# Optimization experiments

Measured on AMD Instinct MI355X. Metric: run time of the kernel, lower is better.

The kernel has to match this reference:

```python
import jax, jax.numpy as jnp
import numpy as np


def _cdist(x, y):
    # Euclidean (L2) distance matrix, matching torch.cdist default p=2.
    # x: [B,N,D], y: [B,M,D] -> [B,N,M]
    x2 = jnp.sum(x * x, axis=-1, keepdims=True)          # [B,N,1]
    y2 = jnp.sum(y * y, axis=-1, keepdims=True)          # [B,M,1]
    d2 = x2 + jnp.swapaxes(y2, -1, -2) - 2.0 * jnp.einsum('bnd,bmd->bnm', x, y)
    return jnp.sqrt(jnp.maximum(d2, 0.0))


def setup_inputs() -> dict:
    key = jax.random.key(0)
    k1, k2, k3 = jax.random.split(key, 3)
    B, N, G, D = 1, 8192, 2048, 64
    expression = jax.random.normal(k1, (B, N, G), dtype=jnp.float32)
    encoding = jax.random.normal(k2, (B, N, D), dtype=jnp.float32)
    quality = jax.random.normal(k3, (B, N, 1), dtype=jnp.float32)
    return {"expression": expression, "encoding": encoding, "quality": quality}


def reference(expression, encoding, quality):
    # scores[b,i,j] = -||enc_i - enc_j|| + quality[b,j]
    scores = -_cdist(encoding, encoding) + jnp.swapaxes(quality, -1, -2)  # [B,N,N]
    similarity = jax.nn.softmax(scores, axis=-1)
    return similarity @ expression  # [B,N,G]
```

## Files before the change

### kernel.cpp

```cpp
#include <hip/hip_runtime.h>
#include <hip/hip_bf16.h>


typedef __attribute__((ext_vector_type(8))) short bf16x8;
typedef __attribute__((ext_vector_type(4))) float f32x4;
typedef __attribute__((ext_vector_type(16))) float f32x16;

constexpr int N_ = 8192;
constexpr int G_ = 2048;
constexpr int D_ = 64;

__device__ __forceinline__ unsigned short f32_to_bf16(float f) {
  unsigned u = __builtin_bit_cast(unsigned, f);
  u = (u + 0x7FFFu + ((u >> 16) & 1u)) >> 16;
  return (unsigned short)u;
}
__device__ __forceinline__ float bf16_to_f32(unsigned short h) {
  unsigned u = ((unsigned)h) << 16;
  return __builtin_bit_cast(float, u);
}

typedef __attribute__((address_space(1))) const unsigned int glob_u32;
typedef __attribute__((address_space(3))) unsigned int lds_u32;
__device__ __forceinline__ void gload_lds16(const void* g, void* l) {
  __builtin_amdgcn_global_load_lds((glob_u32*)g, (lds_u32*)l, 16, 0, 0);
}

__global__ void prep_kernel(const float* __restrict__ enc,
                            const float* __restrict__ quality,
                            float* __restrict__ norms,
                            float2* __restrict__ nq,
                            unsigned short* __restrict__ encb) {
  int row = blockIdx.x * blockDim.x + threadIdx.x;
  if (row >= N_) return;
  const float* r = enc + (size_t)row * D_;
  float n = 0.f;
#pragma unroll
  for (int k = 0; k < D_; k += 4) {
    float4 v = *(const float4*)(r + k);
    n += v.x * v.x + v.y * v.y + v.z * v.z + v.w * v.w;
    ushort4 h;
    h.x = f32_to_bf16(v.x); h.y = f32_to_bf16(v.y);
    h.z = f32_to_bf16(v.z); h.w = f32_to_bf16(v.w);
    *(ushort4*)(encb + (size_t)row * D_ + k) = h;
  }
  norms[row] = n;
  nq[row] = make_float2(n, quality[row]);
}

__global__ void etrans_kernel(const float* __restrict__ E,
                              unsigned short* __restrict__ ET) {
  __shared__ __align__(16) unsigned short t[64 * 72];
  int j0 = blockIdx.x * 64;
  int g0 = blockIdx.y * 64;
  int tid = threadIdx.x;
#pragma unroll
  for (int it = 0; it < 4; ++it) {
    int r = it * 16 + (tid >> 4);
    int c4 = tid & 15;
    float4 v = *(const float4*)(E + (size_t)(j0 + r) * G_ + g0 + c4 * 4);
    t[(c4 * 4 + 0) * 72 + r] = f32_to_bf16(v.x);
    t[(c4 * 4 + 1) * 72 + r] = f32_to_bf16(v.y);
    t[(c4 * 4 + 2) * 72 + r] = f32_to_bf16(v.z);
    t[(c4 * 4 + 3) * 72 + r] = f32_to_bf16(v.w);
  }
  __syncthreads();
#pragma unroll
  for (int it = 0; it < 2; ++it) {
    int g = it * 32 + (tid >> 3);
    int ch = tid & 7;
    bf16x8 v = *(const bf16x8*)(&t[g * 72 + ch * 8]);
    *(bf16x8*)(ET + (size_t)(g0 + g) * N_ + j0 + ch * 8) = v;
  }
}

__global__ __launch_bounds__(256)
void pk_kernel(const unsigned short* __restrict__ encb,
               const float* __restrict__ norms,
               const float2* __restrict__ nq,
               unsigned short* __restrict__ P,
               float* __restrict__ lpart) {
  __shared__ __align__(16) unsigned short p_lds[64 * 72];

  const int tid = threadIdx.x;
  const int wave = tid >> 6;
  const int lane = tid & 63;
  const int quad = lane >> 4;
  const int l15 = lane & 15;

  const int i0 = blockIdx.y * 64;
  const int jbase = blockIdx.x * 1024;
  const int irow_a = i0 + 16 * wave + l15;
  const int iloc_c = 16 * wave + quad * 4;
  const int irow_c = i0 + iloc_c;

  const int srow_loc = 16 * wave + (lane >> 2);

  bf16x8 afrag[2];
#pragma unroll
  for (int ks = 0; ks < 2; ++ks)
    afrag[ks] = *(const bf16x8*)(encb + (size_t)irow_a * 64 + ks * 32 + quad * 8);

  float ni[4];
#pragma unroll
  for (int r = 0; r < 4; ++r) ni[r] = norms[irow_c + r];

  float lsum[4] = {0.f, 0.f, 0.f, 0.f};

  for (int js = 0; js < 16; ++js) {
    const int j0j = jbase + js * 64;
#pragma unroll
    for (int jt = 0; jt < 4; ++jt) {
      const int jrow = j0j + jt * 16 + l15;
      bf16x8 b0 = *(const bf16x8*)(encb + (size_t)jrow * 64 + quad * 8);
      bf16x8 b1 = *(const bf16x8*)(encb + (size_t)jrow * 64 + 32 + quad * 8);
      float2 njq = nq[jrow];
      f32x4 s4 = {0.f, 0.f, 0.f, 0.f};
      s4 = __builtin_amdgcn_mfma_f32_16x16x32_bf16(afrag[0], b0, s4, 0, 0, 0);
      s4 = __builtin_amdgcn_mfma_f32_16x16x32_bf16(afrag[1], b1, s4, 0, 0, 0);
#pragma unroll
      for (int r = 0; r < 4; ++r) {
        float d2 = fmaxf(ni[r] + njq.x - 2.0f * s4[r], 0.f);
        float sc = njq.y - sqrtf(d2);
        if (irow_c + r == jrow) sc = njq.y;
        float p = __expf(sc);
        unsigned short pb = f32_to_bf16(p);
        lsum[r] += bf16_to_f32(pb);
        p_lds[(iloc_c + r) * 72 + jt * 16 + l15] = pb;
      }
    }
    __syncthreads();
#pragma unroll
    for (int k = 0; k < 2; ++k) {
      int c = (lane & 3) + k * 4;
      bf16x8 v = *(const bf16x8*)(&p_lds[srow_loc * 72 + c * 8]);
      *(bf16x8*)(P + (size_t)(i0 + srow_loc) * N_ + j0j + c * 8) = v;
    }
    __syncthreads();
  }
#pragma unroll
  for (int r = 0; r < 4; ++r) {
    float v = lsum[r];
    v += __shfl_xor(v, 1);
    v += __shfl_xor(v, 2);
    v += __shfl_xor(v, 4);
    v += __shfl_xor(v, 8);
    lsum[r] = v;
  }
  if (l15 == 0) {
#pragma unroll
    for (int r = 0; r < 4; ++r)
      lpart[(size_t)blockIdx.x * N_ + irow_c + r] = lsum[r];
  }
}

__global__ void inv_kernel(const float* __restrict__ lpart,
                           float* __restrict__ linv) {
  int i = blockIdx.x * blockDim.x + threadIdx.x;
  if (i >= N_) return;
  float s = 0.f;
#pragma unroll
  for (int c = 0; c < 8; ++c) s += lpart[(size_t)c * N_ + i];
  linv[i] = 1.0f / s;
}

__global__ __launch_bounds__(256, 2)
void gemm_kernel(const unsigned short* __restrict__ P,
                 const unsigned short* __restrict__ ET,
                 const float* __restrict__ linv,
                 float* __restrict__ out) {
  __shared__ __align__(16) unsigned short aT[256 * 64];
  __shared__ __align__(16) unsigned short bT[128 * 64];

  const int tid = threadIdx.x;
  const int wave = tid >> 6;
  const int lane = tid & 63;
  const int quad = lane >> 4;
  const int l15 = lane & 15;

  const int g0 = blockIdx.x * 128;
  const int i0 = blockIdx.y * 256;
  const int wrow = (wave >> 1) * 128;
  const int wcol = (wave & 1) * 64;

  const int strow = tid >> 3;
  const int stc = tid & 7;

  f32x4 acc[8][4];
#pragma unroll
  for (int a = 0; a < 8; ++a)
#pragma unroll
    for (int b = 0; b < 4; ++b) acc[a][b] = (f32x4){0.f, 0.f, 0.f, 0.f};

  for (int kk = 0; kk < N_; kk += 64) {
#pragma unroll
    for (int s = 0; s < 8; ++s) {
      int row = s * 32 + strow;
      int csrc = stc ^ (row & 7);
      gload_lds16(P + (size_t)(i0 + row) * N_ + kk + csrc * 8,
                  &aT[row * 64 + stc * 8]);
    }
#pragma unroll
    for (int s = 0; s < 4; ++s) {
      int row = s * 32 + strow;
      int csrc = stc ^ (row & 7);
      gload_lds16(ET + (size_t)(g0 + row) * N_ + kk + csrc * 8,
                  &bT[row * 64 + stc * 8]);
    }
    __syncthreads();
#pragma unroll
    for (int ks = 0; ks < 2; ++ks) {
      const int swzk = ((ks * 4 + quad) ^ (l15 & 7)) * 8;
      bf16x8 bF[4];
#pragma unroll
      for (int ct = 0; ct < 4; ++ct)
        bF[ct] = *(const bf16x8*)(&bT[(wcol + ct * 16 + l15) * 64 + swzk]);
#pragma unroll
      for (int rt = 0; rt < 8; ++rt) {
        bf16x8 aF = *(const bf16x8*)(&aT[(wrow + rt * 16 + l15) * 64 + swzk]);
#pragma unroll
        for (int ct = 0; ct < 4; ++ct)
          acc[rt][ct] = __builtin_amdgcn_mfma_f32_16x16x32_bf16(aF, bF[ct], acc[rt][ct], 0, 0, 0);
      }
    }
    __syncthreads();
  }

  float li[8];
#pragma unroll
  for (int rt = 0; rt < 8; ++rt) {
    li[rt] = 0.f;
  }
#pragma unroll
  for (int rt = 0; rt < 8; ++rt) {
    float lir[4];
#pragma unroll
    for (int r = 0; r < 4; ++r)
      lir[r] = linv[i0 + wrow + rt * 16 + quad * 4 + r];
#pragma unroll
    for (int ct = 0; ct < 4; ++ct)
#pragma unroll
      for (int r = 0; r < 4; ++r) {
        int row = wrow + rt * 16 + quad * 4 + r;
        int col = wcol + ct * 16 + l15;
        out[(size_t)(i0 + row) * G_ + g0 + col] = acc[rt][ct][r] * lir[r];
      }
  }
}

__global__ __launch_bounds__(256, 2)
void fused_kernel(const unsigned short* __restrict__ encb,
                  const float* __restrict__ norms,
                  const float2* __restrict__ nq,
                  const unsigned short* __restrict__ ET,
                  float* __restrict__ out) {
  __shared__ __align__(16) unsigned short p_lds[128 * 72];
  __shared__ __align__(16) unsigned short e_lds[256 * 72];
  __shared__ float linv_lds[128];

  const int tid = threadIdx.x;
  const int wave = tid >> 6;
  const int lane = tid & 63;
  const int quad = lane >> 4;
  const int l15 = lane & 15;
  const int half = lane >> 5;
  const int l31 = lane & 31;

  const int gt = blockIdx.x & 7;
  const int it = blockIdx.x >> 3;
  const int i0 = it * 128;
  const int g0 = gt * 256;

  const int srow = 32 * wave;
  const int wr = wave >> 1, wc = wave & 1;
  const int prow = 64 * wr;
  const int pcol = 128 * wc;

  bf16x8 afrag[2][2];
#pragma unroll
  for (int rt = 0; rt < 2; ++rt)
#pragma unroll
    for (int ks = 0; ks < 2; ++ks)
      afrag[rt][ks] = *(const bf16x8*)(encb +
          (size_t)(i0 + srow + rt * 16 + l15) * 64 + ks * 32 + quad * 8);

  float ni[2][4];
#pragma unroll
  for (int rt = 0; rt < 2; ++rt)
#pragma unroll
    for (int r = 0; r < 4; ++r)
      ni[rt][r] = norms[i0 + srow + rt * 16 + quad * 4 + r];

  float lsum[2][4] = {};
  f32x16 acc[2][4];
#pragma unroll
  for (int a = 0; a < 2; ++a)
#pragma unroll
    for (int b = 0; b < 4; ++b)
#pragma unroll
      for (int e = 0; e < 16; ++e) acc[a][b][e] = 0.f;

  for (int j0j = 0; j0j < N_; j0j += 64) {
#pragma unroll
    for (int s = 0; s < 8; ++s) {
      int g = s * 32 + (tid >> 3);
      int ch = tid & 7;
      bf16x8 v = *(const bf16x8*)(ET + (size_t)(g0 + g) * N_ + j0j + ch * 8);
      *(bf16x8*)(&e_lds[g * 72 + ch * 8]) = v;
    }
#pragma unroll
    for (int jt = 0; jt < 4; ++jt) {
      const int jrow = j0j + jt * 16 + l15;
      bf16x8 b0 = *(const bf16x8*)(encb + (size_t)jrow * 64 + quad * 8);
      bf16x8 b1 = *(const bf16x8*)(encb + (size_t)jrow * 64 + 32 + quad * 8);
      float2 njq = nq[jrow];
#pragma unroll
      for (int rt = 0; rt < 2; ++rt) {
        f32x4 s4 = {0.f, 0.f, 0.f, 0.f};
        s4 = __builtin_amdgcn_mfma_f32_16x16x32_bf16(afrag[rt][0], b0, s4, 0, 0, 0);
        s4 = __builtin_amdgcn_mfma_f32_16x16x32_bf16(afrag[rt][1], b1, s4, 0, 0, 0);
#pragma unroll
        for (int r = 0; r < 4; ++r) {
          int i_loc = srow + rt * 16 + quad * 4 + r;
          float d2 = fmaxf(ni[rt][r] + njq.x - 2.0f * s4[r], 0.f);
          float sc = njq.y - sqrtf(d2);
          if (i0 + i_loc == jrow) sc = njq.y;
          float p = __expf(sc);
          unsigned short pb = f32_to_bf16(p);
          lsum[rt][r] += bf16_to_f32(pb);
          p_lds[i_loc * 72 + jt * 16 + l15] = pb;
        }
      }
    }
    __syncthreads();
#pragma unroll
    for (int ks = 0; ks < 4; ++ks) {
      bf16x8 pa0 = *(const bf16x8*)(&p_lds[(prow + l31) * 72 + ks * 16 + half * 8]);
      bf16x8 pa1 = *(const bf16x8*)(&p_lds[(prow + 32 + l31) * 72 + ks * 16 + half * 8]);
#pragma unroll
      for (int ct = 0; ct < 4; ++ct) {
        bf16x8 eb = *(const bf16x8*)(&e_lds[(pcol + ct * 32 + l31) * 72 + ks * 16 + half * 8]);
        acc[0][ct] = __builtin_amdgcn_mfma_f32_32x32x16_bf16(pa0, eb, acc[0][ct], 0, 0, 0);
        acc[1][ct] = __builtin_amdgcn_mfma_f32_32x32x16_bf16(pa1, eb, acc[1][ct], 0, 0, 0);
      }
    }
    __syncthreads();
  }

#pragma unroll
  for (int rt = 0; rt < 2; ++rt)
#pragma unroll
    for (int r = 0; r < 4; ++r) {
      float v = lsum[rt][r];
      v += __shfl_xor(v, 1);
      v += __shfl_xor(v, 2);
      v += __shfl_xor(v, 4);
      v += __shfl_xor(v, 8);
      lsum[rt][r] = v;
    }
  if (l15 == 0) {
#pragma unroll
    for (int rt = 0; rt < 2; ++rt)
#pragma unroll
      for (int r = 0; r < 4; ++r)
        linv_lds[srow + rt * 16 + quad * 4 + r] = 1.0f / lsum[rt][r];
  }
  __syncthreads();

#pragma unroll
  for (int rt2 = 0; rt2 < 2; ++rt2)
#pragma unroll
    for (int ct = 0; ct < 4; ++ct)
#pragma unroll
      for (int e = 0; e < 16; ++e) {
        int row = prow + rt2 * 32 + (e & 3) + 8 * (e >> 2) + 4 * half;
        int col = pcol + ct * 32 + l31;
        out[(size_t)(i0 + row) * G_ + g0 + col] = acc[rt2][ct][e] * linv_lds[row];
      }
}

extern "C" void kernel_launch(void* const* d_in, const int* in_sizes, int n_in,
                              void* d_out, int out_size, void* d_ws, size_t ws_size,
                              hipStream_t stream) {
  const float* expr = (const float*)d_in[0];
  const float* enc  = (const float*)d_in[1];
  const float* qual = (const float*)d_in[2];
  float* out = (float*)d_out;

  char* ws = (char*)d_ws;
  const size_t off_norms = 0;
  const size_t off_nq    = 32768;
  const size_t off_lpart = 98304;
  const size_t off_linv  = 360448;
  const size_t off_encb  = 393216;
  const size_t off_ET    = 1441792;
  const size_t off_P     = 34996224;
  const size_t need      = off_P + (size_t)N_ * N_ * 2;

  if (ws_size >= need) {
    float* norms         = (float*)(ws + off_norms);
    float2* nqp          = (float2*)(ws + off_nq);
    float* lpart         = (float*)(ws + off_lpart);
    float* linv          = (float*)(ws + off_linv);
    unsigned short* encb = (unsigned short*)(ws + off_encb);
    unsigned short* ET   = (unsigned short*)(ws + off_ET);
    unsigned short* P    = (unsigned short*)(ws + off_P);

    prep_kernel<<<dim3(N_ / 256), dim3(256), 0, stream>>>(enc, qual, norms, nqp, encb);
    etrans_kernel<<<dim3(N_ / 64, G_ / 64), dim3(256), 0, stream>>>(expr, ET);
    pk_kernel<<<dim3(8, N_ / 64), dim3(256), 0, stream>>>(encb, norms, nqp, P, lpart);
    inv_kernel<<<dim3(N_ / 256), dim3(256), 0, stream>>>(lpart, linv);
    gemm_kernel<<<dim3(G_ / 128, N_ / 256), dim3(256), 0, stream>>>(P, ET, linv, out);
  } else {
    float* norms         = (float*)ws;
    float2* nqp          = (float2*)(ws + 32768);
    unsigned short* encb = (unsigned short*)(ws + 98304);
    unsigned short* ET   = (unsigned short*)(ws + 1146880);
    prep_kernel<<<dim3(N_ / 256), dim3(256), 0, stream>>>(enc, qual, norms, nqp, encb);
    etrans_kernel<<<dim3(N_ / 64, G_ / 64), dim3(256), 0, stream>>>(expr, ET);
    fused_kernel<<<dim3((N_ / 128) * (G_ / 256)), dim3(256), 0, stream>>>(encb, norms, nqp, ET, out);
  }
}
```

Measured before the change: 429.6 us.

## Add 256x256-tile 8-wave GEMM with triple-buffered LDS pipeline and swizzled block order

```diff
diff --git a/kernel.cpp b/kernel.cpp
--- a/kernel.cpp
+++ b/kernel.cpp
@@ -164,6 +164,147 @@
   linv[i] = 1.0f / s;
 }
 
+constexpr int GBM = 256, GBN = 256, GBK = 32;
+constexpr int GNT = N_ / GBK;
+constexpr int SLOT_A = GBM * GBK;
+constexpr int SLOT_B = GBN * GBK;
+constexpr int SLOT = SLOT_A + SLOT_B;
+constexpr int GEMM_LDS_BYTES = 3 * SLOT * 2;
+
+__global__ __launch_bounds__(512, 2)
+void gemm8_kernel(const unsigned short* __restrict__ P,
+                  const unsigned short* __restrict__ ET,
+                  const float* __restrict__ linv,
+                  float* __restrict__ out) {
+  extern __shared__ __align__(16) unsigned short smem[];
+
+  const int tid = threadIdx.x;
+  const int wave = tid >> 6;
+  const int lane = tid & 63;
+  const int quad = lane >> 4;
+  const int l15 = lane & 15;
+
+  const int bid = blockIdx.x;
+  const int lg = (bid & 7) * 32 + (bid >> 3);
+  const int gx = lg & 7;
+  const int gy = lg >> 3;
+  const int g0 = gx * GBN;
+  const int i0 = gy * GBM;
+
+  const int wm = wave >> 2;
+  const int wn = wave & 3;
+  const int wrow = wm * 128;
+  const int wcol = wn * 64;
+
+  unsigned short* cur = smem;
+  unsigned short* nxt = smem + SLOT;
+  unsigned short* stg = smem + 2 * SLOT;
+
+  const int strow = tid >> 2;
+  const int stch = tid & 3;
+  const int rowS0 = strow, rowS1 = 128 + strow;
+  const int cs0 = stch ^ ((rowS0 >> 1) & 3);
+  const int cs1 = stch ^ ((rowS1 >> 1) & 3);
+  const int dA0 = rowS0 * GBK + stch * 8;
+  const int dA1 = rowS1 * GBK + stch * 8;
+  const int dB0 = SLOT_A + rowS0 * GBK + stch * 8;
+  const int dB1 = SLOT_A + rowS1 * GBK + stch * 8;
+  const unsigned short* pA0 = P + (size_t)(i0 + rowS0) * N_ + cs0 * 8;
+  const unsigned short* pA1 = P + (size_t)(i0 + rowS1) * N_ + cs1 * 8;
+  const unsigned short* pB0 = ET + (size_t)(g0 + rowS0) * N_ + cs0 * 8;
+  const unsigned short* pB1 = ET + (size_t)(g0 + rowS1) * N_ + cs1 * 8;
+
+  int offA0[4], offA1[4], offB[4];
+#pragma unroll
+  for (int r = 0; r < 4; ++r) {
+    int rowh0 = wrow + r * 16 + l15;
+    int rowh1 = wrow + 64 + r * 16 + l15;
+    offA0[r] = rowh0 * GBK + (quad ^ ((rowh0 >> 1) & 3)) * 8;
+    offA1[r] = rowh1 * GBK + (quad ^ ((rowh1 >> 1) & 3)) * 8;
+    int rowb = wcol + r * 16 + l15;
+    offB[r] = SLOT_A + rowb * GBK + (quad ^ ((rowb >> 1) & 3)) * 8;
+  }
+
+  f32x4 acc[8][4];
+#pragma unroll
+  for (int a = 0; a < 8; ++a)
+#pragma unroll
+    for (int b = 0; b < 4; ++b) acc[a][b] = (f32x4){0.f, 0.f, 0.f, 0.f};
+
+  gload_lds16(pA0, cur + dA0);
+  gload_lds16(pA1, cur + dA1);
+  gload_lds16(pB0, cur + dB0);
+  gload_lds16(pB1, cur + dB1);
+  gload_lds16(pA0 + GBK, nxt + dA0);
+  gload_lds16(pA1 + GBK, nxt + dA1);
+  gload_lds16(pB0 + GBK, nxt + dB0);
+  gload_lds16(pB1 + GBK, nxt + dB1);
+  pA0 += 2 * GBK; pA1 += 2 * GBK; pB0 += 2 * GBK; pB1 += 2 * GBK;
+  asm volatile("s_waitcnt vmcnt(4)" ::: "memory");
+  __builtin_amdgcn_s_barrier();
+
+  bf16x8 aF[4], bF[4];
+  for (int u = 0; u < GNT; ++u) {
+    const bool do_stage = (u + 2 < GNT);
+    __builtin_amdgcn_sched_barrier(0);
+#pragma unroll
+    for (int r = 0; r < 4; ++r) bF[r] = *(const bf16x8*)(cur + offB[r]);
+#pragma unroll
+    for (int r = 0; r < 4; ++r) aF[r] = *(const bf16x8*)(cur + offA0[r]);
+    if (do_stage) {
+      gload_lds16(pA0, stg + dA0);
+      gload_lds16(pA1, stg + dA1);
+    }
+    __builtin_amdgcn_s_barrier();
+    __builtin_amdgcn_s_setprio(1);
+#pragma unroll
+    for (int r = 0; r < 4; ++r)
+#pragma unroll
+      for (int c = 0; c < 4; ++c)
+        acc[r][c] = __builtin_amdgcn_mfma_f32_16x16x32_bf16(aF[r], bF[c], acc[r][c], 0, 0, 0);
+    __builtin_amdgcn_s_setprio(0);
+    __builtin_amdgcn_s_barrier();
+#pragma unroll
+    for (int r = 0; r < 4; ++r) aF[r] = *(const bf16x8*)(cur + offA1[r]);
+    if (do_stage) {
+      gload_lds16(pB0, stg + dB0);
+      gload_lds16(pB1, stg + dB1);
+    }
+    __builtin_amdgcn_s_barrier();
+    __builtin_amdgcn_s_setprio(1);
+#pragma unroll
+    for (int r = 0; r < 4; ++r)
+#pragma unroll
+      for (int c = 0; c < 4; ++c)
+        acc[4 + r][c] = __builtin_amdgcn_mfma_f32_16x16x32_bf16(aF[r], bF[c], acc[4 + r][c], 0, 0, 0);
+    __builtin_amdgcn_s_setprio(0);
+    if (do_stage) {
+      asm volatile("s_waitcnt vmcnt(4)" ::: "memory");
+    } else {
+      asm volatile("s_waitcnt vmcnt(0)" ::: "memory");
+    }
+    __builtin_amdgcn_s_barrier();
+    pA0 += GBK; pA1 += GBK; pB0 += GBK; pB1 += GBK;
+    unsigned short* tmp = cur; cur = nxt; nxt = stg; stg = tmp;
+  }
+
+#pragma unroll
+  for (int rt = 0; rt < 8; ++rt) {
+    float lir[4];
+#pragma unroll
+    for (int r = 0; r < 4; ++r)
+      lir[r] = linv[i0 + wrow + rt * 16 + quad * 4 + r];
+#pragma unroll
+    for (int ct = 0; ct < 4; ++ct)
+#pragma unroll
+      for (int r = 0; r < 4; ++r) {
+        int row = wrow + rt * 16 + quad * 4 + r;
+        int col = wcol + ct * 16 + l15;
+        out[(size_t)(i0 + row) * G_ + g0 + col] = acc[rt][ct][r] * lir[r];
+      }
+  }
+}
+
 __global__ __launch_bounds__(256, 2)
 void gemm_kernel(const unsigned short* __restrict__ P,
                  const unsigned short* __restrict__ ET,
@@ -226,11 +367,6 @@
     __syncthreads();
   }
 
-  float li[8];
-#pragma unroll
-  for (int rt = 0; rt < 8; ++rt) {
-    li[rt] = 0.f;
-  }
 #pragma unroll
   for (int rt = 0; rt < 8; ++rt) {
     float lir[4];
@@ -397,6 +533,16 @@
   const size_t off_P     = 34996224;
   const size_t need      = off_P + (size_t)N_ * N_ * 2;
 
+  static bool smem_init = false;
+  static bool smem_ok = false;
+  if (!smem_init) {
+    smem_init = true;
+    hipError_t e = hipFuncSetAttribute(
+        reinterpret_cast<const void*>(gemm8_kernel),
+        hipFuncAttributeMaxDynamicSharedMemorySize, GEMM_LDS_BYTES);
+    smem_ok = (e == hipSuccess);
+  }
+
   if (ws_size >= need) {
     float* norms         = (float*)(ws + off_norms);
     float2* nqp          = (float2*)(ws + off_nq);
@@ -410,7 +556,12 @@
     etrans_kernel<<<dim3(N_ / 64, G_ / 64), dim3(256), 0, stream>>>(expr, ET);
     pk_kernel<<<dim3(8, N_ / 64), dim3(256), 0, stream>>>(encb, norms, nqp, P, lpart);
     inv_kernel<<<dim3(N_ / 256), dim3(256), 0, stream>>>(lpart, linv);
-    gemm_kernel<<<dim3(G_ / 128, N_ / 256), dim3(256), 0, stream>>>(P, ET, linv, out);
+    if (smem_ok) {
+      gemm8_kernel<<<dim3((N_ / GBM) * (G_ / GBN)), dim3(512), GEMM_LDS_BYTES, stream>>>(
+          P, ET, linv, out);
+    } else {
+      gemm_kernel<<<dim3(G_ / 128, N_ / 256), dim3(256), 0, stream>>>(P, ET, linv, out);
+    }
   } else {
     float* norms         = (float*)ws;
     float2* nqp          = (float2*)(ws + 32768);
```

Result: no change. 425.9 us (-0.9%).
